# Optimization experiments

Hardware: AMD Instinct MI355X
Metric: run time of the kernel (lower is better)

Reference implementation:

```python
import jax, jax.numpy as jnp
import numpy as np

D = 128          # embed_dim
NSYM = 100000    # num_symbols
PAD = NSYM       # padding idx (zero row)
B = 2048         # query batch
FEW = 5          # support set size
M = 128          # max neighbors
KTAB = 64        # knn table width
K = 32           # knn_k topk
STEPS = 4        # process_steps
DM = 2 * D       # d_model for encoders (256)
HID = 2 * DM     # LSTM hidden (512)


def _cos(a, b):
    # torch F.cosine_similarity, eps=1e-8; a [B,1,d], b [B,N,d] -> [B,N]
    num = jnp.sum(a * b, axis=-1)
    den = jnp.maximum(jnp.linalg.norm(a, axis=-1) * jnp.linalg.norm(b, axis=-1), 1e-8)
    return num / den


def _l2n(x):
    return x / jnp.maximum(jnp.linalg.norm(x, axis=-1, keepdims=True), 1e-12)


def _neighbor_encoder(conn, ids, knn_tab, emb, gcn_w, gcn_w_b, gcn_b, gate_w, gate_b):
    rel = emb[conn[..., 0]]                      # [N,M,D]
    ent = emb[conn[..., 1]]                      # [N,M,D]
    center = emb[ids][:, None, :]                # [N,1,D]
    sim = _cos(center, ent)                      # [N,M]
    _, idx = jax.lax.top_k(sim, K)               # [N,K]
    rel_k = jnp.take_along_axis(rel, idx[..., None], axis=1)
    ent_k = jnp.take_along_axis(ent, idx[..., None], axis=1)
    h = jnp.concatenate([rel_k, ent_k], axis=-1) @ gcn_w.T + gcn_w_b + gcn_b
    struct = jnp.tanh(h.mean(axis=1))            # [N,D]
    # knn branch: gather knn neighbor ids, cosine topk, pad-relation embeds (zero row)
    kent = emb[knn_tab[ids]]                     # [N,KTAB,D]
    sim2 = _cos(center, kent)
    _, idx2 = jax.lax.top_k(sim2, K)
    kent_k = jnp.take_along_axis(kent, idx2[..., None], axis=1)
    pad_row = jax.lax.stop_gradient(emb[PAD])    # padding_idx row (zeros, no grad)
    krel = jnp.broadcast_to(pad_row, kent_k.shape)
    h2 = jnp.concatenate([krel, kent_k], axis=-1) @ gcn_w.T + gcn_w_b + gcn_b
    knn_mean = jnp.tanh(h2.mean(axis=1))         # [N,D]
    alpha = jax.nn.sigmoid(jnp.concatenate([struct, knn_mean], axis=-1) @ gate_w.T + gate_b)
    return (1.0 - alpha) * struct + alpha * knn_mean


def _support_encoder(x, p1_w, p1_b, p2_w, p2_b, ln_g, ln_b):
    o = jax.nn.relu(x @ p1_w.T + p1_b) @ p2_w.T + p2_b
    z = o + x
    mu = z.mean(axis=-1, keepdims=True)
    sig = z.std(axis=-1, ddof=1, keepdims=True)  # torch unbiased std
    return (z - mu) / (sig + 1e-3) * ln_g + ln_b


def _query_encoder(support, query, w_ih, w_hh, b_ih, b_hh):
    # attLSTM processing block; support [1,DM], query [B,DM]
    n = query.shape[0]
    h_r = jnp.zeros((n, HID), query.dtype)
    c = jnp.zeros((n, HID), query.dtype)
    h = query
    for _ in range(STEPS):
        g = query @ w_ih.T + b_ih + h_r @ w_hh.T + b_hh
        i, f, gg, o = jnp.split(g, 4, axis=-1)
        c = jax.nn.sigmoid(f) * c + jax.nn.sigmoid(i) * jnp.tanh(gg)
        h_ = jax.nn.sigmoid(o) * jnp.tanh(c)
        h = query + h_[:, :DM]
        attn = jax.nn.softmax(h @ support.T, axis=1)  # [B,1]
        r = attn @ support                             # [B,DM]
        h_r = jnp.concatenate([h, r], axis=1)
    return h


def _forward(query, support, q_l_conn, q_r_conn, s_l_conn, s_r_conn, knn_neighbors,
             emb, gcn_w, gcn_w_b, gcn_b, gate_w, gate_b,
             p1_w, p1_b, p2_w, p2_b, ln_g, ln_b, w_ih, w_hh, b_ih, b_hh):
    ne = lambda conn, ids: _neighbor_encoder(conn, ids, knn_neighbors, emb,
                                             gcn_w, gcn_w_b, gcn_b, gate_w, gate_b)
    ql = ne(q_l_conn, query[:, 0])
    qr = ne(q_r_conn, query[:, 1])
    sl = ne(s_l_conn, support[:, 0])
    sr = ne(s_r_conn, support[:, 1])
    qn = jnp.concatenate([ql, qr], axis=-1)   # [B,DM]
    sn = jnp.concatenate([sl, sr], axis=-1)   # [FEW,DM]
    se = lambda x: _support_encoder(x, p1_w, p1_b, p2_w, p2_b, ln_g, ln_b)
    support_g = se(sn).mean(axis=0, keepdims=True)  # [1,DM]
    query_g = se(qn)                                 # [B,DM]
    query_f = _l2n(_query_encoder(support_g, query_g, w_ih, w_hh, b_ih, b_hh))
    sg = _l2n(support_g[0])
    return query_f @ sg                              # [B]


def setup_inputs() -> dict:
    key = jax.random.key(0)
    ks = jax.random.split(key, 24)
    f = lambda i, shape, s=0.05: jax.random.normal(ks[i], shape, dtype=jnp.float32) * s
    ri = lambda i, shape: jax.random.randint(ks[i], shape, 0, NSYM).astype(jnp.int32)
    emb = f(0, (NSYM + 1, D), 0.5).at[PAD].set(0.0)
    return dict(
        query=ri(1, (B, 2)), support=ri(2, (FEW, 2)),
        q_l_conn=ri(3, (B, M, 2)),
        q_l_deg=jax.random.randint(ks[4], (B,), 1, M).astype(jnp.int32),
        q_r_conn=ri(5, (B, M, 2)),
        q_r_deg=jax.random.randint(ks[6], (B,), 1, M).astype(jnp.int32),
        s_l_conn=ri(7, (FEW, M, 2)),
        s_l_deg=jax.random.randint(ks[8], (FEW,), 1, M).astype(jnp.int32),
        s_r_conn=ri(9, (FEW, M, 2)),
        s_r_deg=jax.random.randint(ks[10], (FEW,), 1, M).astype(jnp.int32),
        knn_neighbors=ri(11, (NSYM + 1, KTAB)),
        emb=emb,
        gcn_w=f(12, (D, 2 * D)), gcn_w_b=f(13, (D,)),
        gcn_b=jnp.zeros((D,), jnp.float32),
        gate_w=f(14, (1, 2 * D)), gate_b=jnp.zeros((1,), jnp.float32),
        p1_w=f(15, (2 * DM, DM)), p1_b=f(16, (2 * DM,)),
        p2_w=f(17, (DM, 2 * DM)), p2_b=f(18, (DM,)),
        ln_g=jnp.ones((DM,), jnp.float32), ln_b=jnp.zeros((DM,), jnp.float32),
        w_ih=f(19, (4 * HID, DM)), w_hh=f(20, (4 * HID, HID)),
        b_ih=f(21, (4 * HID,)), b_hh=f(22, (4 * HID,)),
    )


def reference(query, support, q_l_conn, q_l_deg, q_r_conn, q_r_deg,
              s_l_conn, s_l_deg, s_r_conn, s_r_deg, knn_neighbors,
              emb, gcn_w, gcn_w_b, gcn_b, gate_w, gate_b,
              p1_w, p1_b, p2_w, p2_b, ln_g, ln_b, w_ih, w_hh, b_ih, b_hh):
    # degrees are computed-but-unused in this fork's neighbor_encoder (plain mean)
    return _forward(query, support, q_l_conn, q_r_conn, s_l_conn, s_r_conn, knn_neighbors,
                    emb, gcn_w, gcn_w_b, gcn_b, gate_w, gate_b,
                    p1_w, p1_b, p2_w, p2_b, ln_g, ln_b, w_ih, w_hh, b_ih, b_hh)
```

## Files before the change

kernel.cpp:

```cpp
#include <hip/hip_runtime.h>
#include <hip/hip_bf16.h>

typedef unsigned short u16;
typedef unsigned int u32;

constexpr int ED   = 128;
constexpr int MC   = 128;
constexpr int KT   = 64;
constexpr int KS   = 32;
constexpr int NB   = 2048;
constexpr int NF   = 5;
constexpr int DMM  = 256;
constexpr int NG   = 1024;
constexpr int PADID = 100000;

typedef __attribute__((ext_vector_type(8))) short short8;
typedef __attribute__((ext_vector_type(4))) float floatx4;

__device__ __forceinline__ float bf2f(u16 u){
  union { u32 i; float f; } v; v.i = ((u32)u) << 16; return v.f;
}
__device__ __forceinline__ float lo2f(u32 w){
  union { u32 i; float f; } v; v.i = w << 16; return v.f;
}
__device__ __forceinline__ float hi2f(u32 w){
  union { u32 i; float f; } v; v.i = w & 0xffff0000u; return v.f;
}
__device__ __forceinline__ u16 f2bf(float f){
  union { float f; u32 i; } v; v.f = f;
  u32 r = v.i + 0x7FFFu + ((v.i >> 16) & 1u);
  return (u16)(r >> 16);
}
__device__ __forceinline__ float sigf(float x){ return 1.f / (1.f + expf(-x)); }

__device__ __forceinline__ float gld(const void* p, size_t i, bool bf){
  return bf ? bf2f(((const u16*)p)[i]) : ((const float*)p)[i];
}
__device__ __forceinline__ void ld2(const void* p, size_t i0, bool bf, float* o){
  if (bf){ u32 w = *(const u32*)((const u16*)p + i0); o[0]=lo2f(w); o[1]=hi2f(w); }
  else   { float2 v = *(const float2*)((const float*)p + i0); o[0]=v.x; o[1]=v.y; }
}
__device__ __forceinline__ void ld4(const void* p, size_t i0, bool bf, float* o){
  if (bf){ uint2 w = *(const uint2*)((const u16*)p + i0);
           o[0]=lo2f(w.x); o[1]=hi2f(w.x); o[2]=lo2f(w.y); o[3]=hi2f(w.y); }
  else   { float4 v = *(const float4*)((const float*)p + i0);
           o[0]=v.x; o[1]=v.y; o[2]=v.z; o[3]=v.w; }
}
__device__ __forceinline__ void ld8(const void* p, size_t i0, bool bf, float* o){
  if (bf){
    uint4 v = *(const uint4*)((const u16*)p + i0);
    o[0]=lo2f(v.x); o[1]=hi2f(v.x); o[2]=lo2f(v.y); o[3]=hi2f(v.y);
    o[4]=lo2f(v.z); o[5]=hi2f(v.z); o[6]=lo2f(v.w); o[7]=hi2f(v.w);
  } else {
    const float* f = (const float*)p + i0;
    float4 a = *(const float4*)f, b = *(const float4*)(f + 4);
    o[0]=a.x; o[1]=a.y; o[2]=a.z; o[3]=a.w; o[4]=b.x; o[5]=b.y; o[6]=b.z; o[7]=b.w;
  }
}
__device__ __forceinline__ float dotw(const void* w, size_t i0, const float* x, int n, bool bf){
  float acc = 0.f, t[8];
  #pragma unroll 4
  for (int j = 0; j < n; j += 8){
    ld8(w, i0 + j, bf, t);
    #pragma unroll
    for (int q = 0; q < 8; q++) acc += t[q]*x[j+q];
  }
  return acc;
}

__device__ __forceinline__ float waveSum(float v){
  #pragma unroll
  for (int o = 32; o > 0; o >>= 1) v += __shfl_xor(v, o, 64);
  return v;
}
__device__ __forceinline__ float blockSum(float v, float* s8){
  int lane = threadIdx.x & 63, wid = threadIdx.x >> 6;
  v = waveSum(v);
  __syncthreads();
  if (lane == 0) s8[wid] = v;
  __syncthreads();
  return s8[0] + s8[1] + s8[2] + s8[3];
}
__device__ __forceinline__ float2 blockSum2(float a, float b, float* s8){
  int lane = threadIdx.x & 63, wid = threadIdx.x >> 6;
  a = waveSum(a); b = waveSum(b);
  __syncthreads();
  if (lane == 0){ s8[wid] = a; s8[4 + wid] = b; }
  __syncthreads();
  float2 r;
  r.x = s8[0] + s8[1] + s8[2] + s8[3];
  r.y = s8[4] + s8[5] + s8[6] + s8[7];
  return r;
}

__global__ void sniff_kernel(const void* ln_g, int* flag){
  if (threadIdx.x == 0 && blockIdx.x == 0)
    *flag = (*(const u32*)ln_g == 0x3F803F80u) ? 1 : 0;
}

__global__ __launch_bounds__(256) void neighbor_kernel(
    const int* __restrict__ query, const int* __restrict__ support,
    const int* __restrict__ qlc, const int* __restrict__ qrc,
    const int* __restrict__ slc, const int* __restrict__ srcc,
    const int* __restrict__ knnt, const void* __restrict__ emb,
    const void* __restrict__ gcn_w, const void* __restrict__ gcn_w_b,
    const void* __restrict__ gcn_b, const void* __restrict__ gate_w,
    const void* __restrict__ gate_b,
    float* __restrict__ qn, float* __restrict__ sn, const int* __restrict__ flag)
{
  const bool bf = (*flag != 0);
  int blk = blockIdx.x;
  const int* conn; int id; float* outp;
  if (blk < NB)            { id = query[2*blk];                 conn = qlc + (size_t)blk*MC*2;  outp = qn + (size_t)blk*DMM; }
  else if (blk < 2*NB)     { int r = blk - NB;   id = query[2*r+1];   conn = qrc + (size_t)r*MC*2; outp = qn + (size_t)r*DMM + ED; }
  else if (blk < 2*NB+NF)  { int r = blk - 2*NB; id = support[2*r];   conn = slc + (size_t)r*MC*2; outp = sn + (size_t)r*DMM; }
  else                     { int r = blk - 2*NB - NF; id = support[2*r+1]; conn = srcc + (size_t)r*MC*2; outp = sn + (size_t)r*DMM + ED; }

  __shared__ float s_center[ED], s_pad[ED];
  __shared__ float s_sim[256];
  __shared__ float s_meanR[ED], s_meanE[ED], s_meanK[ED];
  __shared__ float s_struct[ED], s_knn[ED];
  __shared__ float s_red[8];
  __shared__ int s_eid[MC + KT];
  __shared__ int s_selE[KS], s_selR[KS], s_selK[KS];

  const int tid = threadIdx.x, lane = tid & 63, wid = tid >> 6;

  if (tid < ED){
    s_center[tid] = gld(emb, (size_t)id*ED + tid, bf);
    s_pad[tid]    = gld(emb, (size_t)PADID*ED + tid, bf);
  }
  if (tid < MC)           s_eid[tid] = conn[2*tid + 1];
  else if (tid < MC + KT) s_eid[tid] = knnt[(size_t)id*KT + (tid - MC)];

  float cpart = 0.f;
  if (tid < ED){ float c = s_center[tid]; cpart = c*c; }
  float cnorm = sqrtf(blockSum(cpart, s_red));

  const int g = lane & 15;
  float creg[8];
  #pragma unroll
  for (int j = 0; j < 8; j++) creg[j] = s_center[g*8 + j];

  #pragma unroll 2
  for (int m0 = wid*4; m0 < MC + KT; m0 += 16){
    int m = m0 + (lane >> 4);
    int eid = s_eid[m];
    float e[8];
    ld8(emb, (size_t)eid*ED + g*8, bf, e);
    float d = 0.f, q = 0.f;
    #pragma unroll
    for (int j = 0; j < 8; j++){ d += creg[j]*e[j]; q += e[j]*e[j]; }
    #pragma unroll
    for (int o = 8; o > 0; o >>= 1){ d += __shfl_xor(d, o, 64); q += __shfl_xor(q, o, 64); }
    if (g == 0) s_sim[m] = d / fmaxf(cnorm * sqrtf(q), 1e-8f);
  }
  __syncthreads();

  if (tid < MC){
    float v = s_sim[tid];
    int cnt = 0;
    for (int j = 0; j < MC; j++){
      float w = s_sim[j];
      cnt += (w > v || (w == v && j < tid)) ? 1 : 0;
    }
    if (cnt < KS){ s_selR[cnt] = conn[2*tid]; s_selE[cnt] = s_eid[tid]; }
  } else if (tid < MC + KT){
    int t = tid - MC;
    float v = s_sim[MC + t];
    int cnt = 0;
    for (int j = 0; j < KT; j++){
      float w = s_sim[MC + j];
      cnt += (w > v || (w == v && j < t)) ? 1 : 0;
    }
    if (cnt < KS) s_selK[cnt] = s_eid[MC + t];
  }
  __syncthreads();

  {
    int dd = tid & (ED - 1);
    float acc = 0.f;
    if (tid < ED){
      #pragma unroll 8
      for (int k = 0; k < KS; k++) acc += gld(emb, (size_t)s_selE[k]*ED + dd, bf);
      s_meanE[dd] = acc * (1.f/KS);
    } else {
      #pragma unroll 8
      for (int k = 0; k < KS; k++) acc += gld(emb, (size_t)s_selR[k]*ED + dd, bf);
      s_meanR[dd] = acc * (1.f/KS);
    }
    float acck = 0.f;
    int half = tid >> 7;
    #pragma unroll 8
    for (int k = 0; k < 16; k++) acck += gld(emb, (size_t)s_selK[half*16 + k]*ED + dd, bf);
    s_sim[tid] = acck;
  }
  __syncthreads();
  if (tid < ED) s_meanK[tid] = (s_sim[tid] + s_sim[tid + 128]) * (1.f/KS);
  __syncthreads();

  {
    int dd = tid & (ED - 1);
    size_t wrow = (size_t)dd * (2*ED);
    float base = gld(gcn_w_b, dd, bf) + gld(gcn_b, dd, bf);
    if (tid < ED){
      float acc = base + dotw(gcn_w, wrow, s_meanR, ED, bf) + dotw(gcn_w, wrow + ED, s_meanE, ED, bf);
      s_struct[dd] = tanhf(acc);
    } else {
      float acc = base + dotw(gcn_w, wrow, s_pad, ED, bf) + dotw(gcn_w, wrow + ED, s_meanK, ED, bf);
      s_knn[dd] = tanhf(acc);
    }
  }
  __syncthreads();
  float gv = 0.f;
  if (tid < ED) gv = gld(gate_w, tid, bf)*s_struct[tid] + gld(gate_w, ED + tid, bf)*s_knn[tid];
  float alpha = sigf(blockSum(gv, s_red) + gld(gate_b, 0, bf));
  if (tid < ED) outp[tid] = (1.f - alpha)*s_struct[tid] + alpha*s_knn[tid];
}

__global__ __launch_bounds__(256) void mlp_enc_kernel(
    const float* __restrict__ src,
    const void* __restrict__ p1_w, const void* __restrict__ p1_b,
    const void* __restrict__ p2_w, const void* __restrict__ p2_b,
    const void* __restrict__ ln_g, const void* __restrict__ ln_b,
    float* __restrict__ dst, int nrows, const int* __restrict__ flag)
{
  const bool bf = (*flag != 0);
  constexpr int RPB = 8;
  __shared__ float x[RPB][DMM];
  __shared__ float hid[RPB][2*DMM];
  __shared__ float s_red[8];
  int tid = threadIdx.x;
  int r0 = blockIdx.x * RPB;
  for (int r = 0; r < RPB; r++)
    x[r][tid] = (r0 + r < nrows) ? src[(size_t)(r0 + r)*DMM + tid] : 0.f;
  __syncthreads();

  {
    float acc0[RPB], acc1[RPB];
    #pragma unroll
    for (int r = 0; r < RPB; r++){ acc0[r] = 0.f; acc1[r] = 0.f; }
    for (int j8 = 0; j8 < DMM/8; j8++){
      float wa[8], wb[8];
      ld8(p1_w, (size_t)tid*DMM + j8*8, bf, wa);
      ld8(p1_w, (size_t)(tid+256)*DMM + j8*8, bf, wb);
      #pragma unroll
      for (int r = 0; r < RPB; r++){
        const float* xr = &x[r][j8*8];
        float s0 = 0.f, s1 = 0.f;
        #pragma unroll
        for (int q = 0; q < 8; q++){ float xv = xr[q]; s0 += wa[q]*xv; s1 += wb[q]*xv; }
        acc0[r] += s0; acc1[r] += s1;
      }
    }
    float bb0 = gld(p1_b, tid, bf), bb1 = gld(p1_b, tid + 256, bf);
    #pragma unroll
    for (int r = 0; r < RPB; r++){
      hid[r][tid]     = fmaxf(acc0[r] + bb0, 0.f);
      hid[r][tid+256] = fmaxf(acc1[r] + bb1, 0.f);
    }
  }
  __syncthreads();

  float zr[RPB];
  {
    #pragma unroll
    for (int r = 0; r < RPB; r++) zr[r] = 0.f;
    for (int j8 = 0; j8 < (2*DMM)/8; j8++){
      float wa[8];
      ld8(p2_w, (size_t)tid*(2*DMM) + j8*8, bf, wa);
      #pragma unroll
      for (int r = 0; r < RPB; r++){
        const float* hr = &hid[r][j8*8];
        float s0 = 0.f;
        #pragma unroll
        for (int q = 0; q < 8; q++) s0 += wa[q]*hr[q];
        zr[r] += s0;
      }
    }
    float bb = gld(p2_b, tid, bf);
    #pragma unroll
    for (int r = 0; r < RPB; r++) zr[r] += bb + x[r][tid];
  }

  float lg = gld(ln_g, tid, bf), lb = gld(ln_b, tid, bf);
  for (int r = 0; r < RPB; r++){
    float2 st = blockSum2(zr[r], zr[r]*zr[r], s_red);
    float mu = st.x * (1.f/DMM);
    float var = (st.y - (float)DMM*mu*mu) * (1.f/(DMM - 1));
    float sig = sqrtf(fmaxf(var, 0.f));
    if (r0 + r < nrows)
      dst[(size_t)(r0 + r)*DMM + tid] = (zr[r] - mu)/(sig + 1e-3f)*lg + lb;
  }
}

__global__ __launch_bounds__(256) void svec_kernel(
    const void* __restrict__ w_hh, const void* __restrict__ b_ih, const void* __restrict__ b_hh,
    const float* __restrict__ seS, float* __restrict__ cvec0, float* __restrict__ svec,
    float* __restrict__ sgn, const int* __restrict__ flag)
{
  const bool bf = (*flag != 0);
  __shared__ float sg[DMM];
  __shared__ float s_red[8];
  int tid = threadIdx.x;
  float a = 0.f;
  for (int r = 0; r < NF; r++) a += seS[r*DMM + tid];
  a *= (1.f/NF);
  sg[tid] = a;
  __syncthreads();
  if (blockIdx.x == 0){
    float nn = blockSum(a*a, s_red);
    sgn[tid] = a / fmaxf(sqrtf(nn), 1e-12f);
  }
  int u = blockIdx.x * 256 + tid;
  int wrow = (u >> 8)*512 + (u & 255);
  cvec0[u] = gld(b_ih, wrow, bf) + gld(b_hh, wrow, bf);
  svec[u] = dotw(w_hh, (size_t)wrow*(2*DMM) + DMM, sg, DMM, bf);
}

__global__ __launch_bounds__(256) void gemm_gates(
    const float* __restrict__ A,
    const void* __restrict__ W, int wstride,
    const float* __restrict__ addvec, const float* __restrict__ addmat,
    float* __restrict__ C, const int* __restrict__ flag)
{
  const bool bf = (*flag != 0);
  int tid = threadIdx.x;
  int n0 = blockIdx.x * 64, m0 = blockIdx.y * 64;

  if (bf){
    constexpr int KP = 136;
    __shared__ u16 As[64 * KP];
    __shared__ u16 Ws[64 * KP];
    const int wv = tid >> 6, lane = tid & 63;
    const int quad = lane >> 4, l16 = lane & 15;
    const int sr = tid >> 5, sc = tid & 31;

    floatx4 acc[4];
    #pragma unroll
    for (int t = 0; t < 4; t++) acc[t] = (floatx4){0.f, 0.f, 0.f, 0.f};

    for (int kc = 0; kc < 256; kc += 128){
      __syncthreads();
      #pragma unroll
      for (int i = 0; i < 8; i++){
        int r = i*8 + sr;
        float4 v = *(const float4*)(A + (size_t)(m0 + r)*256 + kc + sc*4);
        u32 p0 = (u32)f2bf(v.x) | ((u32)f2bf(v.y) << 16);
        u32 p1 = (u32)f2bf(v.z) | ((u32)f2bf(v.w) << 16);
        *(uint2*)&As[r*KP + sc*4] = make_uint2(p0, p1);
      }
      #pragma unroll
      for (int i = 0; i < 8; i++){
        int nn = i*8 + sr;
        int gn = n0 + nn;
        int wrow = (gn >> 8)*512 + (gn & 255);
        uint2 wv2 = *(const uint2*)((const u16*)W + (size_t)wrow*wstride + kc + sc*4);
        *(uint2*)&Ws[nn*KP + sc*4] = wv2;
      }
      __syncthreads();
      int am = wv*16 + l16;
      #pragma unroll
      for (int k1 = 0; k1 < 128; k1 += 32){
        int ko = k1 + quad*8;
        short8 af = *(const short8*)&As[am*KP + ko];
        #pragma unroll
        for (int t = 0; t < 4; t++){
          short8 bfr = *(const short8*)&Ws[(t*16 + l16)*KP + ko];
          acc[t] = __builtin_amdgcn_mfma_f32_16x16x32_bf16(af, bfr, acc[t], 0, 0, 0);
        }
      }
    }

    #pragma unroll
    for (int t = 0; t < 4; t++){
      int col = n0 + t*16 + l16;
      float av = addvec ? addvec[col] : 0.f;
      #pragma unroll
      for (int r = 0; r < 4; r++){
        int row = m0 + wv*16 + quad*4 + r;
        float val = acc[t][r] + av;
        if (addmat) val += addmat[(size_t)row*NG + col];
        C[(size_t)row*NG + col] = val;
      }
    }
    return;
  }

  {
    __shared__ float As2[16][68];
    __shared__ float Ws2[16][68];
    int tx = tid & 15, ty = tid >> 4;
    int sn_ = tid & 63, kq = tid >> 6;
    int gn = n0 + sn_;
    size_t wbase = (size_t)((gn >> 8)*512 + (gn & 255)) * wstride;
    int ar = tid >> 2, ac = (tid & 3) * 4;
    const float* ap = A + (size_t)(m0 + ar)*256 + ac;

    float acc[4][4];
    #pragma unroll
    for (int i = 0; i < 4; i++)
      #pragma unroll
      for (int j = 0; j < 4; j++) acc[i][j] = 0.f;

    for (int kc = 0; kc < 256; kc += 16){
      __syncthreads();
      float4 av = *(const float4*)(ap + kc);
      As2[ac+0][ar] = av.x; As2[ac+1][ar] = av.y; As2[ac+2][ar] = av.z; As2[ac+3][ar] = av.w;
      float wt[4];
      ld4(W, wbase + kc + kq*4, false, wt);
      Ws2[kq*4+0][sn_] = wt[0]; Ws2[kq*4+1][sn_] = wt[1];
      Ws2[kq*4+2][sn_] = wt[2]; Ws2[kq*4+3][sn_] = wt[3];
      __syncthreads();
      #pragma unroll
      for (int k = 0; k < 16; k++){
        float4 a = *(const float4*)&As2[k][ty*4];
        float4 b = *(const float4*)&Ws2[k][tx*4];
        acc[0][0] += a.x*b.x; acc[0][1] += a.x*b.y; acc[0][2] += a.x*b.z; acc[0][3] += a.x*b.w;
        acc[1][0] += a.y*b.x; acc[1][1] += a.y*b.y; acc[1][2] += a.y*b.z; acc[1][3] += a.y*b.w;
        acc[2][0] += a.z*b.x; acc[2][1] += a.z*b.y; acc[2][2] += a.z*b.z; acc[2][3] += a.z*b.w;
        acc[3][0] += a.w*b.x; acc[3][1] += a.w*b.y; acc[3][2] += a.w*b.z; acc[3][3] += a.w*b.w;
      }
    }

    float4 addc = make_float4(0.f, 0.f, 0.f, 0.f);
    if (addvec){
      float4 t = *(const float4*)(addvec + n0 + tx*4);
      addc.x = t.x; addc.y = t.y; addc.z = t.z; addc.w = t.w;
    }
    #pragma unroll
    for (int i = 0; i < 4; i++){
      int row = m0 + ty*4 + i;
      float4 v = make_float4(acc[i][0]+addc.x, acc[i][1]+addc.y, acc[i][2]+addc.z, acc[i][3]+addc.w);
      if (addmat){
        float4 t = *(const float4*)(addmat + (size_t)row*NG + n0 + tx*4);
        v.x += t.x; v.y += t.y; v.z += t.z; v.w += t.w;
      }
      *(float4*)(C + (size_t)row*NG + n0 + tx*4) = v;
    }
  }
}

__global__ __launch_bounds__(256) void lstm_elem(
    const float* __restrict__ g, const float* __restrict__ query_g,
    float* __restrict__ c, float* __restrict__ h, int first,
    const float* __restrict__ sgn, void* __restrict__ out, const int* __restrict__ flag)
{
  __shared__ float s_red[8];
  int b = blockIdx.x, j = threadIdx.x;
  const float* gb = g + (size_t)b*NG;
  float iv = gb[j], fv = gb[256 + j], gv = gb[512 + j], ov = gb[768 + j];
  float cc = first ? 0.f : c[(size_t)b*DMM + j];
  cc = sigf(fv)*cc + sigf(iv)*tanhf(gv);
  c[(size_t)b*DMM + j] = cc;
  float hh = query_g[(size_t)b*DMM + j] + sigf(ov)*tanhf(cc);
  h[(size_t)b*DMM + j] = hh;
  if (out){
    float2 st = blockSum2(hh*sgn[j], hh*hh, s_red);
    if (j == 0){
      float v = st.x / fmaxf(sqrtf(st.y), 1e-12f);
      if (*flag) ((__hip_bfloat16*)out)[b] = __float2bfloat16(v);
      else       ((float*)out)[b] = v;
    }
  }
}

extern "C" void kernel_launch(void* const* d_in, const int* in_sizes, int n_in,
                              void* d_out, int out_size, void* d_ws, size_t ws_size,
                              hipStream_t stream)
{
  const int* query   = (const int*)d_in[0];
  const int* support = (const int*)d_in[1];
  const int* qlc     = (const int*)d_in[2];
  const int* qrc     = (const int*)d_in[4];
  const int* slc     = (const int*)d_in[6];
  const int* srcc    = (const int*)d_in[8];
  const int* knnt    = (const int*)d_in[10];
  const void* emb     = d_in[11];
  const void* gcn_w   = d_in[12];
  const void* gcn_w_b = d_in[13];
  const void* gcn_b   = d_in[14];
  const void* gate_w  = d_in[15];
  const void* gate_b  = d_in[16];
  const void* p1_w    = d_in[17];
  const void* p1_b    = d_in[18];
  const void* p2_w    = d_in[19];
  const void* p2_b    = d_in[20];
  const void* ln_g    = d_in[21];
  const void* ln_b    = d_in[22];
  const void* w_ih    = d_in[23];
  const void* w_hh    = d_in[24];
  const void* b_ih    = d_in[25];
  const void* b_hh    = d_in[26];

  int* flag = (int*)d_ws;
  float* ws = (float*)d_ws + 64;
  size_t off = 0;
  float* qn        = ws + off; off += (size_t)NB*DMM;
  float* sn        = ws + off; off += NF*DMM;
  float* query_g   = ws + off; off += (size_t)NB*DMM;
  float* seS       = ws + off; off += NF*DMM;
  float* sgn       = ws + off; off += DMM;
  float* cvec0     = ws + off; off += NG;
  float* svec      = ws + off; off += NG;
  float* qx        = ws + off; off += (size_t)NB*NG;
  float* gbuf      = ws + off; off += (size_t)NB*NG;
  float* hbuf      = ws + off; off += (size_t)NB*DMM;
  float* cbuf      = ws + off; off += (size_t)NB*DMM;
  (void)sn; (void)seS;

  sniff_kernel<<<1, 64, 0, stream>>>(ln_g, flag);

  neighbor_kernel<<<2*NB + 2*NF, 256, 0, stream>>>(
      query, support, qlc, qrc, slc, srcc, knnt, emb,
      gcn_w, gcn_w_b, gcn_b, gate_w, gate_b, qn, sn, flag);

  mlp_enc_kernel<<<(NB + NF + 7)/8, 256, 0, stream>>>(
      qn, p1_w, p1_b, p2_w, p2_b, ln_g, ln_b, query_g, NB + NF, flag);

  svec_kernel<<<NG/256, 256, 0, stream>>>(w_hh, b_ih, b_hh, seS, cvec0, svec, sgn, flag);

  gemm_gates<<<dim3(NG/64, NB/64), 256, 0, stream>>>(query_g, w_ih, 256, cvec0, nullptr, qx, flag);

  lstm_elem<<<NB, 256, 0, stream>>>(qx, query_g, cbuf, hbuf, 1, nullptr, nullptr, flag);
  for (int s = 1; s < 4; s++){
    gemm_gates<<<dim3(NG/64, NB/64), 256, 0, stream>>>(hbuf, w_hh, 512, svec, qx, gbuf, flag);
    lstm_elem<<<NB, 256, 0, stream>>>(gbuf, query_g, cbuf, hbuf, 0,
                                      sgn, (s == 3) ? d_out : nullptr, flag);
  }

  (void)in_sizes; (void)n_in; (void)out_size; (void)ws_size;
}
```

Baseline: 521.4 us.

## Batch GCN projection into a tiled GEMM across all neighbor rows

```diff
diff --git a/kernel.cpp b/kernel.cpp
--- a/kernel.cpp
+++ b/kernel.cpp
@@ -13,6 +13,9 @@
 constexpr int DMM  = 256;
 constexpr int NG   = 1024;
 constexpr int PADID = 100000;
+constexpr int NROWS = 2*NB + 2*NF;
+constexpr int MT   = (NROWS + 63)/64;
+constexpr int MP   = MT*64;
 
 typedef __attribute__((ext_vector_type(8))) short short8;
 typedef __attribute__((ext_vector_type(4))) float floatx4;
@@ -103,33 +106,26 @@
     const int* __restrict__ qlc, const int* __restrict__ qrc,
     const int* __restrict__ slc, const int* __restrict__ srcc,
     const int* __restrict__ knnt, const void* __restrict__ emb,
-    const void* __restrict__ gcn_w, const void* __restrict__ gcn_w_b,
-    const void* __restrict__ gcn_b, const void* __restrict__ gate_w,
-    const void* __restrict__ gate_b,
-    float* __restrict__ qn, float* __restrict__ sn, const int* __restrict__ flag)
+    float* __restrict__ gA, float* __restrict__ gK, const int* __restrict__ flag)
 {
   const bool bf = (*flag != 0);
   int blk = blockIdx.x;
-  const int* conn; int id; float* outp;
-  if (blk < NB)            { id = query[2*blk];                 conn = qlc + (size_t)blk*MC*2;  outp = qn + (size_t)blk*DMM; }
-  else if (blk < 2*NB)     { int r = blk - NB;   id = query[2*r+1];   conn = qrc + (size_t)r*MC*2; outp = qn + (size_t)r*DMM + ED; }
-  else if (blk < 2*NB+NF)  { int r = blk - 2*NB; id = support[2*r];   conn = slc + (size_t)r*MC*2; outp = sn + (size_t)r*DMM; }
-  else                     { int r = blk - 2*NB - NF; id = support[2*r+1]; conn = srcc + (size_t)r*MC*2; outp = sn + (size_t)r*DMM + ED; }
-
-  __shared__ float s_center[ED], s_pad[ED];
-  __shared__ float s_sim[256];
-  __shared__ float s_meanR[ED], s_meanE[ED], s_meanK[ED];
-  __shared__ float s_struct[ED], s_knn[ED];
+  const int* conn; int id;
+  if (blk < NB)            { id = query[2*blk];                 conn = qlc + (size_t)blk*MC*2; }
+  else if (blk < 2*NB)     { int r = blk - NB;   id = query[2*r+1];   conn = qrc + (size_t)r*MC*2; }
+  else if (blk < 2*NB+NF)  { int r = blk - 2*NB; id = support[2*r];   conn = slc + (size_t)r*MC*2; }
+  else                     { int r = blk - 2*NB - NF; id = support[2*r+1]; conn = srcc + (size_t)r*MC*2; }
+
+  __shared__ float s_center[ED];
+  __shared__ float s_sim[MC + KT];
   __shared__ float s_red[8];
   __shared__ int s_eid[MC + KT];
   __shared__ int s_selE[KS], s_selR[KS], s_selK[KS];
+  __shared__ float s_mt[3][8][ED];
 
   const int tid = threadIdx.x, lane = tid & 63, wid = tid >> 6;
 
-  if (tid < ED){
-    s_center[tid] = gld(emb, (size_t)id*ED + tid, bf);
-    s_pad[tid]    = gld(emb, (size_t)PADID*ED + tid, bf);
-  }
+  if (tid < ED) s_center[tid] = gld(emb, (size_t)id*ED + tid, bf);
   if (tid < MC)           s_eid[tid] = conn[2*tid + 1];
   else if (tid < MC + KT) s_eid[tid] = knnt[(size_t)id*KT + (tid - MC)];
 
@@ -142,7 +138,7 @@
   #pragma unroll
   for (int j = 0; j < 8; j++) creg[j] = s_center[g*8 + j];
 
-  #pragma unroll 2
+  #pragma unroll 4
   for (int m0 = wid*4; m0 < MC + KT; m0 += 16){
     int m = m0 + (lane >> 4);
     int eid = s_eid[m];
@@ -160,6 +156,7 @@
   if (tid < MC){
     float v = s_sim[tid];
     int cnt = 0;
+    #pragma unroll 8
     for (int j = 0; j < MC; j++){
       float w = s_sim[j];
       cnt += (w > v || (w == v && j < tid)) ? 1 : 0;
@@ -169,6 +166,7 @@
     int t = tid - MC;
     float v = s_sim[MC + t];
     int cnt = 0;
+    #pragma unroll 8
     for (int j = 0; j < KT; j++){
       float w = s_sim[MC + j];
       cnt += (w > v || (w == v && j < t)) ? 1 : 0;
@@ -178,44 +176,128 @@
   __syncthreads();
 
   {
-    int dd = tid & (ED - 1);
-    float acc = 0.f;
+    const int slot = tid >> 5, c4 = (tid & 31)*4;
+    float aR[4] = {0,0,0,0}, aE[4] = {0,0,0,0}, aK[4] = {0,0,0,0};
+    #pragma unroll
+    for (int k = 0; k < 4; k++){
+      float t[4];
+      ld4(emb, (size_t)s_selR[k*8 + slot]*ED + c4, bf, t);
+      aR[0]+=t[0]; aR[1]+=t[1]; aR[2]+=t[2]; aR[3]+=t[3];
+      ld4(emb, (size_t)s_selE[k*8 + slot]*ED + c4, bf, t);
+      aE[0]+=t[0]; aE[1]+=t[1]; aE[2]+=t[2]; aE[3]+=t[3];
+      ld4(emb, (size_t)s_selK[k*8 + slot]*ED + c4, bf, t);
+      aK[0]+=t[0]; aK[1]+=t[1]; aK[2]+=t[2]; aK[3]+=t[3];
+    }
+    *(float4*)&s_mt[0][slot][c4] = make_float4(aR[0], aR[1], aR[2], aR[3]);
+    *(float4*)&s_mt[1][slot][c4] = make_float4(aE[0], aE[1], aE[2], aE[3]);
+    *(float4*)&s_mt[2][slot][c4] = make_float4(aK[0], aK[1], aK[2], aK[3]);
+  }
+  __syncthreads();
+  {
+    int dd = tid & (ED - 1), which = tid >> 7;
+    float s = 0.f;
+    #pragma unroll
+    for (int p = 0; p < 8; p++) s += s_mt[which][p][dd];
+    gA[(size_t)blk*DMM + which*ED + dd] = s * (1.f/KS);
     if (tid < ED){
-      #pragma unroll 8
-      for (int k = 0; k < KS; k++) acc += gld(emb, (size_t)s_selE[k]*ED + dd, bf);
-      s_meanE[dd] = acc * (1.f/KS);
-    } else {
-      #pragma unroll 8
-      for (int k = 0; k < KS; k++) acc += gld(emb, (size_t)s_selR[k]*ED + dd, bf);
-      s_meanR[dd] = acc * (1.f/KS);
-    }
-    float acck = 0.f;
-    int half = tid >> 7;
-    #pragma unroll 8
-    for (int k = 0; k < 16; k++) acck += gld(emb, (size_t)s_selK[half*16 + k]*ED + dd, bf);
-    s_sim[tid] = acck;
-  }
-  __syncthreads();
-  if (tid < ED) s_meanK[tid] = (s_sim[tid] + s_sim[tid + 128]) * (1.f/KS);
-  __syncthreads();
-
-  {
-    int dd = tid & (ED - 1);
-    size_t wrow = (size_t)dd * (2*ED);
-    float base = gld(gcn_w_b, dd, bf) + gld(gcn_b, dd, bf);
-    if (tid < ED){
-      float acc = base + dotw(gcn_w, wrow, s_meanR, ED, bf) + dotw(gcn_w, wrow + ED, s_meanE, ED, bf);
-      s_struct[dd] = tanhf(acc);
-    } else {
-      float acc = base + dotw(gcn_w, wrow, s_pad, ED, bf) + dotw(gcn_w, wrow + ED, s_meanK, ED, bf);
-      s_knn[dd] = tanhf(acc);
-    }
-  }
-  __syncthreads();
-  float gv = 0.f;
-  if (tid < ED) gv = gld(gate_w, tid, bf)*s_struct[tid] + gld(gate_w, ED + tid, bf)*s_knn[tid];
-  float alpha = sigf(blockSum(gv, s_red) + gld(gate_b, 0, bf));
-  if (tid < ED) outp[tid] = (1.f - alpha)*s_struct[tid] + alpha*s_knn[tid];
+      float sk = 0.f;
+      #pragma unroll
+      for (int p = 0; p < 8; p++) sk += s_mt[2][p][dd];
+      gK[(size_t)blk*ED + dd] = sk * (1.f/KS);
+    }
+  }
+}
+
+__global__ __launch_bounds__(256) void gcn_gemm(
+    const float* __restrict__ ARE, const float* __restrict__ AK,
+    const void* __restrict__ gcn_w, const void* __restrict__ gcn_w_b,
+    const void* __restrict__ gcn_b, float* __restrict__ C, const int* __restrict__ flag)
+{
+  const bool bf = (*flag != 0);
+  __shared__ float As2[16][68];
+  __shared__ float Ws2[16][68];
+  int tid = threadIdx.x;
+  int n0 = blockIdx.x * 64;
+  int mt = blockIdx.y;
+  const float* A; int lda, K, woff; size_t cbase; int mtt;
+  if (mt < MT){ A = ARE; lda = DMM; K = DMM; woff = 0;  cbase = 0;              mtt = mt; }
+  else        { A = AK;  lda = ED;  K = ED;  woff = ED; cbase = (size_t)MP*ED;  mtt = mt - MT; }
+  int m0 = mtt*64;
+
+  int tx = tid & 15, ty = tid >> 4;
+  int sn_ = tid & 63, kq = tid >> 6;
+  size_t wbase = (size_t)(n0 + sn_)*DMM + woff;
+  int ar = tid >> 2, ac = (tid & 3)*4;
+  const float* ap = A + (size_t)(m0 + ar)*lda + ac;
+
+  float acc[4][4];
+  #pragma unroll
+  for (int i = 0; i < 4; i++)
+    #pragma unroll
+    for (int j = 0; j < 4; j++) acc[i][j] = 0.f;
+
+  for (int kc = 0; kc < K; kc += 16){
+    __syncthreads();
+    float4 av = *(const float4*)(ap + kc);
+    As2[ac+0][ar] = av.x; As2[ac+1][ar] = av.y; As2[ac+2][ar] = av.z; As2[ac+3][ar] = av.w;
+    float wt[4];
+    ld4(gcn_w, wbase + kc + kq*4, bf, wt);
+    Ws2[kq*4+0][sn_] = wt[0]; Ws2[kq*4+1][sn_] = wt[1];
+    Ws2[kq*4+2][sn_] = wt[2]; Ws2[kq*4+3][sn_] = wt[3];
+    __syncthreads();
+    #pragma unroll
+    for (int k = 0; k < 16; k++){
+      float4 a = *(const float4*)&As2[k][ty*4];
+      float4 b = *(const float4*)&Ws2[k][tx*4];
+      acc[0][0] += a.x*b.x; acc[0][1] += a.x*b.y; acc[0][2] += a.x*b.z; acc[0][3] += a.x*b.w;
+      acc[1][0] += a.y*b.x; acc[1][1] += a.y*b.y; acc[1][2] += a.y*b.z; acc[1][3] += a.y*b.w;
+      acc[2][0] += a.z*b.x; acc[2][1] += a.z*b.y; acc[2][2] += a.z*b.z; acc[2][3] += a.z*b.w;
+      acc[3][0] += a.w*b.x; acc[3][1] += a.w*b.y; acc[3][2] += a.w*b.z; acc[3][3] += a.w*b.w;
+    }
+  }
+
+  float b4[4];
+  #pragma unroll
+  for (int j = 0; j < 4; j++){
+    int n = n0 + tx*4 + j;
+    b4[j] = gld(gcn_w_b, n, bf) + gld(gcn_b, n, bf);
+  }
+  #pragma unroll
+  for (int i = 0; i < 4; i++){
+    int row = m0 + ty*4 + i;
+    float4 v = make_float4(acc[i][0]+b4[0], acc[i][1]+b4[1], acc[i][2]+b4[2], acc[i][3]+b4[3]);
+    *(float4*)(C + cbase + (size_t)row*ED + n0 + tx*4) = v;
+  }
+}
+
+__global__ __launch_bounds__(256) void gcn_epilogue(
+    const float* __restrict__ C, const void* __restrict__ gate_w,
+    const void* __restrict__ gate_b, float* __restrict__ qn,
+    float* __restrict__ sn, const int* __restrict__ flag)
+{
+  const bool bf = (*flag != 0);
+  int wv = threadIdx.x >> 6, lane = threadIdx.x & 63;
+  int r = blockIdx.x*4 + wv;
+  if (r >= NROWS) return;
+  const float* c1 = C + (size_t)r*ED;
+  const float* c2 = C + (size_t)(MP + r)*ED;
+  float2 sv = *(const float2*)(c1 + 2*lane);
+  float2 kv = *(const float2*)(c2 + 2*lane);
+  float s0 = tanhf(sv.x), s1 = tanhf(sv.y);
+  float k0 = tanhf(kv.x), k1 = tanhf(kv.y);
+  float gv = gld(gate_w, 2*lane, bf)*s0 + gld(gate_w, 2*lane+1, bf)*s1
+           + gld(gate_w, ED + 2*lane, bf)*k0 + gld(gate_w, ED + 2*lane+1, bf)*k1;
+  gv = waveSum(gv);
+  float alpha = sigf(gv + gld(gate_b, 0, bf));
+  float* outp;
+  if (r < NB)             outp = qn + (size_t)r*DMM;
+  else if (r < 2*NB)      outp = qn + (size_t)(r - NB)*DMM + ED;
+  else if (r < 2*NB + NF) outp = sn + (size_t)(r - 2*NB)*DMM;
+  else                    outp = sn + (size_t)(r - 2*NB - NF)*DMM + ED;
+  float2 o;
+  o.x = (1.f - alpha)*s0 + alpha*k0;
+  o.y = (1.f - alpha)*s1 + alpha*k1;
+  *(float2*)(outp + 2*lane) = o;
 }
 
 __global__ __launch_bounds__(256) void mlp_enc_kernel(
@@ -507,13 +589,19 @@
   float* gbuf      = ws + off; off += (size_t)NB*NG;
   float* hbuf      = ws + off; off += (size_t)NB*DMM;
   float* cbuf      = ws + off; off += (size_t)NB*DMM;
+  float* gA        = ws + off; off += (size_t)MP*DMM;
+  float* gK        = ws + off; off += (size_t)MP*ED;
+  float* gC        = ws + off; off += (size_t)2*MP*ED;
   (void)sn; (void)seS;
 
   sniff_kernel<<<1, 64, 0, stream>>>(ln_g, flag);
 
-  neighbor_kernel<<<2*NB + 2*NF, 256, 0, stream>>>(
-      query, support, qlc, qrc, slc, srcc, knnt, emb,
-      gcn_w, gcn_w_b, gcn_b, gate_w, gate_b, qn, sn, flag);
+  neighbor_kernel<<<NROWS, 256, 0, stream>>>(
+      query, support, qlc, qrc, slc, srcc, knnt, emb, gA, gK, flag);
+
+  gcn_gemm<<<dim3(2, 2*MT), 256, 0, stream>>>(gA, gK, gcn_w, gcn_w_b, gcn_b, gC, flag);
+
+  gcn_epilogue<<<(NROWS + 3)/4, 256, 0, stream>>>(gC, gate_w, gate_b, qn, sn, flag);
 
   mlp_enc_kernel<<<(NB + NF + 7)/8, 256, 0, stream>>>(
       qn, p1_w, p1_b, p2_w, p2_b, ln_g, ln_b, query_g, NB + NF, flag);
```

New measurement: 434.1 us. 16.7% less time.
